# Kernel tuning notes

Measured on AMD Instinct MI355X. Metric: run time of the kernel, lower is better.

## Reference

```python
import jax, jax.numpy as jnp
import numpy as np

S, B, D_MODEL, H, DH = 2048, 2, 1024, 16, 64
FACTOR = 1.0 / np.sqrt(DH).astype(np.float32)


def setup_inputs() -> dict:
    key = jax.random.key(0)
    ks = jax.random.split(key, 12)
    sc = 0.02
    inp = {
        'query': jax.random.normal(ks[0], (S, B, D_MODEL), jnp.float32),
        'key': jax.random.normal(ks[1], (S, B, D_MODEL), jnp.float32),
        'value': jax.random.normal(ks[2], (S, B, D_MODEL), jnp.float32),
        # causal mask [seq_q, seq_k, 1]; 0 -> masked
        'mask': jnp.tril(jnp.ones((S, S), dtype=bool))[:, :, None],
        'Wq': jax.random.normal(ks[3], (H * DH, D_MODEL), jnp.float32) * sc,
        'bq': jnp.zeros((H * DH,), jnp.float32),
        'Wk': jax.random.normal(ks[4], (H * DH, D_MODEL), jnp.float32) * sc,
        'bk': jnp.zeros((H * DH,), jnp.float32),
        'Wv': jax.random.normal(ks[5], (H * DH, D_MODEL), jnp.float32) * sc,
        'bv': jnp.zeros((H * DH,), jnp.float32),
        'Wo': jax.random.normal(ks[6], (D_MODEL, H * DH), jnp.float32) * sc,
        'bo': jnp.zeros((D_MODEL,), jnp.float32),
    }
    return inp


def _split_heads(x):
    # pattern: 's b (head_dim head_num) -> s b head_num head_dim' (head_dim is OUTER)
    s, b, _ = x.shape
    return x.reshape(s, b, DH, H).transpose(0, 1, 3, 2)  # [s,b,H,DH]


def reference(query, key, value, mask, Wq, bq, Wk, bk, Wv, bv, Wo, bo):
    q = _split_heads(query @ Wq.T + bq)
    k = _split_heads(key @ Wk.T + bk)
    v = _split_heads(value @ Wv.T + bv)
    scores = jnp.einsum('ibhd,jbhd->ijbh', q, k) * FACTOR  # [i,j,b,h]
    scores = jnp.where(mask[..., None], scores, -jnp.inf)
    attn = jax.nn.softmax(scores, axis=1)  # softmax over keys (dim=1)
    out = jnp.einsum('ijbh,jbhd->ibhd', attn, v)  # [i,b,h,d]
    out = out.reshape(S, B, H * DH)  # 'i b h d -> i b (h d)'
    return out @ Wo.T + bo
```

## Files before the change

kernel.cpp:

```cpp
#include <hip/hip_runtime.h>


typedef float f32x4 __attribute__((ext_vector_type(4)));
typedef float f32x16 __attribute__((ext_vector_type(16)));
typedef __bf16 bf16x8_t __attribute__((ext_vector_type(8)));
typedef unsigned short ushort8 __attribute__((ext_vector_type(8)));
typedef unsigned int uint4v __attribute__((ext_vector_type(4)));
typedef unsigned int uint2v __attribute__((ext_vector_type(2)));

#define S_LEN 2048
#define BATCH 2
#define DMODEL 1024
#define NHEAD 16
#define DHEAD 64
#define K_SCALE 0.18033688011112042f
#define NCHUNK 51

__device__ __forceinline__ unsigned short f2bf(float x) {
  unsigned int u = __builtin_bit_cast(unsigned int, x);
  u += 0x7fffu + ((u >> 16) & 1u);
  return (unsigned short)(u >> 16);
}

__device__ __forceinline__ f32x4 mfma16(ushort8 a, ushort8 b, f32x4 c) {
  return __builtin_amdgcn_mfma_f32_16x16x32_bf16(
      __builtin_bit_cast(bf16x8_t, a), __builtin_bit_cast(bf16x8_t, b), c, 0, 0, 0);
}
__device__ __forceinline__ f32x16 mfma32(ushort8 a, ushort8 b, f32x16 c) {
  return __builtin_amdgcn_mfma_f32_32x32x16_bf16(
      __builtin_bit_cast(bf16x8_t, a), __builtin_bit_cast(bf16x8_t, b), c, 0, 0, 0);
}

__device__ __forceinline__ float max3f(float a, float b, float c) {
  return fmaxf(fmaxf(a, b), c);
}

__device__ __forceinline__ ushort8 pack8(float4 a, float4 b, float s) {
  ushort8 t;
  t[0] = f2bf(a.x * s); t[1] = f2bf(a.y * s); t[2] = f2bf(a.z * s); t[3] = f2bf(a.w * s);
  t[4] = f2bf(b.x * s); t[5] = f2bf(b.y * s); t[6] = f2bf(b.z * s); t[7] = f2bf(b.w * s);
  return t;
}

__device__ __forceinline__ void gload16(unsigned short* lds, const unsigned short* g) {
  __builtin_amdgcn_global_load_lds(
      (const __attribute__((address_space(1))) unsigned int*)g,
      (__attribute__((address_space(3))) unsigned int*)lds, 16, 0, 0);
}

__global__ __launch_bounds__(256) void cvt_kernel(
    const float* __restrict__ q, const float* __restrict__ k, const float* __restrict__ v,
    const float* __restrict__ wq, const float* __restrict__ wk,
    const float* __restrict__ wv, const float* __restrict__ wo,
    unsigned short* __restrict__ qB, unsigned short* __restrict__ kB,
    unsigned short* __restrict__ vB, unsigned short* __restrict__ wqB,
    unsigned short* __restrict__ wkB, unsigned short* __restrict__ wvB,
    unsigned short* __restrict__ woB)
{
  const int c = blockIdx.x * 256 + threadIdx.x;
  const float* s; unsigned short* d; int base;
  if      (c < 524288)  { s = q;  d = qB;  base = 0; }
  else if (c < 1048576) { s = k;  d = kB;  base = 524288; }
  else if (c < 1572864) { s = v;  d = vB;  base = 1048576; }
  else if (c < 1703936) { s = wq; d = wqB; base = 1572864; }
  else if (c < 1835008) { s = wk; d = wkB; base = 1703936; }
  else if (c < 1966080) { s = wv; d = wvB; base = 1835008; }
  else                  { s = wo; d = woB; base = 1966080; }
  const size_t off = (size_t)(c - base) * 8;
  const float4 v0 = *reinterpret_cast<const float4*>(s + off);
  const float4 v1 = *reinterpret_cast<const float4*>(s + off + 4);
  *reinterpret_cast<ushort8*>(d + off) = pack8(v0, v1, 1.0f);
}

__global__ __launch_bounds__(256) void gemm_qkv_kernel(
    const unsigned short* __restrict__ qA, const unsigned short* __restrict__ kA,
    const unsigned short* __restrict__ vA,
    const unsigned short* __restrict__ wqW, const unsigned short* __restrict__ wkW,
    const unsigned short* __restrict__ wvW,
    const float* __restrict__ bq, const float* __restrict__ bk,
    const float* __restrict__ bv,
    unsigned short* __restrict__ Cq, unsigned short* __restrict__ Ck,
    unsigned short* __restrict__ Cv)
{
  __shared__ __align__(16) unsigned short As[2][128 * 64];
  __shared__ __align__(16) unsigned short Ws[2][64 * 64];
  const int z = blockIdx.z;
  const unsigned short* A = (z == 0) ? qA : (z == 1) ? kA : vA;
  const unsigned short* W = (z == 0) ? wqW : (z == 1) ? wkW : wvW;
  const float* bias = (z == 0) ? bq : (z == 1) ? bk : bv;
  unsigned short* C = (z == 0) ? Cq : (z == 1) ? Ck : Cv;
  const float oscale = (z == 1) ? K_SCALE : 1.0f;

  const int tid = threadIdx.x;
  const int lane = tid & 63;
  const int w = tid >> 6;
  const int wm = (w >> 1) * 64, wn = (w & 1) * 32;
  const int g = lane >> 4, lr = lane & 15;

  const int bid = (int)blockIdx.x;
  const int widx = (bid & 7) * 64 + (bid >> 3);
  const int n0 = (widx & 15) * 64;
  const int m0 = (widx >> 4) * 128;

  f32x4 acc[4][2] = {};

#define STAGE(buf, k0)                                                              \
  {                                                                                 \
    _Pragma("unroll")                                                               \
    for (int ii = 0; ii < 4; ++ii) {                                                \
      const int c = ii * 256 + tid;                                                 \
      const int row = c >> 3;                                                       \
      const int sl = (c & 7) ^ (row & 7);                                           \
      gload16(&As[buf][c * 8], A + (size_t)(m0 + row) * DMODEL + (k0) + sl * 8);    \
    }                                                                               \
    _Pragma("unroll")                                                               \
    for (int ii = 0; ii < 2; ++ii) {                                                \
      const int c = ii * 256 + tid;                                                 \
      const int row = c >> 3;                                                       \
      const int sl = (c & 7) ^ (row & 7);                                           \
      gload16(&Ws[buf][c * 8], W + (size_t)(n0 + row) * DMODEL + (k0) + sl * 8);    \
    }                                                                               \
  }

  STAGE(0, 0);
  int cur = 0;

  for (int t = 0; t < 16; ++t) {
    __syncthreads();
    if (t < 15) STAGE(cur ^ 1, (t + 1) * 64);

    const char* ab = (const char*)&As[cur][0];
    const char* wb = (const char*)&Ws[cur][0];
#pragma unroll
    for (int kk = 0; kk < 2; ++kk) {
      ushort8 af[4], bw[2];
#pragma unroll
      for (int mt = 0; mt < 4; ++mt) {
        const int row = wm + mt * 16 + lr;
        af[mt] = *reinterpret_cast<const ushort8*>(
            ab + row * 128 + (((kk * 4 + g) ^ (row & 7)) << 4));
      }
#pragma unroll
      for (int nt = 0; nt < 2; ++nt) {
        const int row = wn + nt * 16 + lr;
        bw[nt] = *reinterpret_cast<const ushort8*>(
            wb + row * 128 + (((kk * 4 + g) ^ (row & 7)) << 4));
      }
      __builtin_amdgcn_s_setprio(1);
#pragma unroll
      for (int mt = 0; mt < 4; ++mt)
#pragma unroll
        for (int nt = 0; nt < 2; ++nt)
          acc[mt][nt] = mfma16(af[mt], bw[nt], acc[mt][nt]);
      __builtin_amdgcn_s_setprio(0);
    }
    cur ^= 1;
  }
#undef STAGE

  __syncthreads();
  unsigned short* T = &As[0][0];
#pragma unroll
  for (int nt = 0; nt < 2; ++nt) {
    const int col = n0 + wn + nt * 16 + lr;
    const float bvv = bias[col];
#pragma unroll
    for (int mt = 0; mt < 4; ++mt)
#pragma unroll
      for (int r = 0; r < 4; ++r) {
        const int lrow = wm + mt * 16 + g * 4 + r;
        T[lrow * 64 + wn + nt * 16 + lr] = f2bf((acc[mt][nt][r] + bvv) * oscale);
      }
  }
  __syncthreads();

  const int dfirst = n0 >> 4;
  if (z < 2) {
#pragma unroll
    for (int it = 0; it < 8; ++it) {
      const int e = it * 256 + tid;
      const int h = e & 15, lrow = e >> 4;
      const int n = m0 + lrow, s = n >> 1, bb = n & 1;
      const unsigned short v0 = T[lrow * 64 + 0 * 16 + h];
      const unsigned short v1 = T[lrow * 64 + 1 * 16 + h];
      const unsigned short v2 = T[lrow * 64 + 2 * 16 + h];
      const unsigned short v3 = T[lrow * 64 + 3 * 16 + h];
      uint2v pk = { (unsigned)v0 | ((unsigned)v1 << 16),
                    (unsigned)v2 | ((unsigned)v3 << 16) };
      *reinterpret_cast<uint2v*>(
          C + ((size_t)(bb * 16 + h) * S_LEN + s) * DHEAD + dfirst) = pk;
    }
  } else {
    const int run = tid >> 1, shalf = tid & 1;
    const int bb = run >> 6, rem = run & 63;
    const int h = rem >> 2, dl = rem & 3;
    const int sbase = (m0 >> 1) + shalf * 32;
    unsigned short vals[32];
#pragma unroll
    for (int i = 0; i < 32; ++i) {
      const int lrow = (shalf * 32 + i) * 2 + bb;
      vals[i] = T[lrow * 64 + dl * 16 + h];
    }
    unsigned short* dstp =
        C + ((size_t)(bb * 16 + h) * DHEAD + dfirst + dl) * S_LEN + sbase;
#pragma unroll
    for (int seg = 0; seg < 4; ++seg) {
      uint4v pk;
#pragma unroll
      for (int j = 0; j < 4; ++j)
        pk[j] = (unsigned)vals[seg * 8 + 2 * j] |
                ((unsigned)vals[seg * 8 + 2 * j + 1] << 16);
      *reinterpret_cast<uint4v*>(dstp + seg * 8) = pk;
    }
  }
}

__global__ __launch_bounds__(256) void gemm_out_kernel(
    const unsigned short* __restrict__ A, const unsigned short* __restrict__ W,
    const float* __restrict__ bias, float* __restrict__ C)
{
  __shared__ __align__(16) unsigned short As[2][128 * 64];
  __shared__ __align__(16) unsigned short Ws[2][64 * 64];
  const int tid = threadIdx.x;
  const int lane = tid & 63;
  const int w = tid >> 6;
  const int wm = (w >> 1) * 64, wn = (w & 1) * 32;
  const int g = lane >> 4, lr = lane & 15;

  const int bid = (int)blockIdx.x;
  const int widx = (bid & 7) * 64 + (bid >> 3);
  const int n0 = (widx & 15) * 64;
  const int m0 = (widx >> 4) * 128;

  f32x4 acc[4][2] = {};

#define STAGE(buf, k0)                                                              \
  {                                                                                 \
    _Pragma("unroll")                                                               \
    for (int ii = 0; ii < 4; ++ii) {                                                \
      const int c = ii * 256 + tid;                                                 \
      const int row = c >> 3;                                                       \
      const int sl = (c & 7) ^ (row & 7);                                           \
      gload16(&As[buf][c * 8], A + (size_t)(m0 + row) * DMODEL + (k0) + sl * 8);    \
    }                                                                               \
    _Pragma("unroll")                                                               \
    for (int ii = 0; ii < 2; ++ii) {                                                \
      const int c = ii * 256 + tid;                                                 \
      const int row = c >> 3;                                                       \
      const int sl = (c & 7) ^ (row & 7);                                           \
      gload16(&Ws[buf][c * 8], W + (size_t)(n0 + row) * DMODEL + (k0) + sl * 8);    \
    }                                                                               \
  }

  STAGE(0, 0);
  int cur = 0;

  for (int t = 0; t < 16; ++t) {
    __syncthreads();
    if (t < 15) STAGE(cur ^ 1, (t + 1) * 64);

    const char* ab = (const char*)&As[cur][0];
    const char* wb = (const char*)&Ws[cur][0];
#pragma unroll
    for (int kk = 0; kk < 2; ++kk) {
      ushort8 af[4], bw[2];
#pragma unroll
      for (int mt = 0; mt < 4; ++mt) {
        const int row = wm + mt * 16 + lr;
        af[mt] = *reinterpret_cast<const ushort8*>(
            ab + row * 128 + (((kk * 4 + g) ^ (row & 7)) << 4));
      }
#pragma unroll
      for (int nt = 0; nt < 2; ++nt) {
        const int row = wn + nt * 16 + lr;
        bw[nt] = *reinterpret_cast<const ushort8*>(
            wb + row * 128 + (((kk * 4 + g) ^ (row & 7)) << 4));
      }
      __builtin_amdgcn_s_setprio(1);
#pragma unroll
      for (int mt = 0; mt < 4; ++mt)
#pragma unroll
        for (int nt = 0; nt < 2; ++nt)
          acc[mt][nt] = mfma16(af[mt], bw[nt], acc[mt][nt]);
      __builtin_amdgcn_s_setprio(0);
    }
    cur ^= 1;
  }
#undef STAGE

#pragma unroll
  for (int nt = 0; nt < 2; ++nt) {
    const int col = n0 + wn + nt * 16 + lr;
    const float bvv = bias[col];
#pragma unroll
    for (int mt = 0; mt < 4; ++mt)
#pragma unroll
      for (int r = 0; r < 4; ++r) {
        const int rowg = m0 + wm + mt * 16 + g * 4 + r;
        C[(size_t)rowg * DMODEL + col] = acc[mt][nt][r] + bvv;
      }
  }
}

__global__ __launch_bounds__(256, 4) void attn_part_kernel(
    const unsigned short* __restrict__ Qh, const unsigned short* __restrict__ Kh,
    const unsigned short* __restrict__ Vh, unsigned short* __restrict__ Opart,
    float* __restrict__ mlbuf)
{
  __shared__ __align__(16) unsigned short Ks[2][64 * 64];
  __shared__ __align__(16) unsigned short Vs[2][64 * 64];

  const int tid = threadIdx.x;
  const int lane = tid & 63;
  const int w = tid >> 6;
  const int ln31 = lane & 31;
  const int hf = lane >> 5;

  const int bid = (int)blockIdx.x;
  const int xcd = bid & 7;
  const int sl8 = bid >> 3;
  const int hb = xcd * 4 + sl8 / NCHUNK;
  const int chunkid = sl8 % NCHUNK;

  int u = chunkid;
  int Q = 0, nc = 1;
  while (u >= nc) { u -= nc; ++Q; nc = Q / 3 + 1; }
  const int c = u;

  const int head = hb & 15, b = hb >> 4;
  const int slot = hb * NCHUNK + chunkid;
  const int t0 = c * 6;
  const int tmax = 2 * Q + 1;
  const int t1 = (tmax < t0 + 5) ? tmax : (t0 + 5);
  const int q0 = Q * 128;

  const size_t hoff = (size_t)(b * NHEAD + head) * (S_LEN * DHEAD);
  const unsigned short* Qg = Qh + hoff;
  const unsigned short* Kg = Kh + hoff;
  const unsigned short* Vg = Vh + hoff;

  const int qwb = q0 + w * 32;
  const int qg = qwb + ln31;

  ushort8 qf[4];
#pragma unroll
  for (int kt = 0; kt < 4; ++kt)
    qf[kt] = *reinterpret_cast<const ushort8*>(Qg + (size_t)qg * DHEAD + kt * 16 + hf * 8);

  f32x16 oa0 = {0}, oa1 = {0};
  float mrun = -1e30f, ssum = 0.f;

#define STAGE(buf, kv)                                                             \
  {                                                                                \
    _Pragma("unroll")                                                              \
    for (int ii = 0; ii < 2; ++ii) {                                               \
      const int c2 = ii * 256 + tid;                                               \
      const int row = c2 >> 3;                                                     \
      const int sl = (c2 & 7) ^ (row & 7);                                         \
      gload16(&Ks[buf][c2 * 8], Kg + (size_t)((kv) + row) * 64 + sl * 8);          \
    }                                                                              \
    _Pragma("unroll")                                                              \
    for (int ii = 0; ii < 2; ++ii) {                                               \
      const int c2 = ii * 256 + tid;                                               \
      const int row = c2 >> 3;                                                     \
      const int sl = (c2 & 7) ^ (row & 7);                                         \
      gload16(&Vs[buf][c2 * 8], Vg + (size_t)row * S_LEN + (kv) + sl * 8);         \
    }                                                                              \
  }

  STAGE(0, t0 * 64);
  int cur = 0;

  const int kb0 = ln31 * 128 + ((hf * 16) ^ ((ln31 & 7) << 4));
  const int kb1 = (32 + ln31) * 128 + ((hf * 16) ^ ((ln31 & 7) << 4));

  for (int t = t0; t <= t1; ++t) {
    const int kv0 = t * 64;
    __syncthreads();
    if (t < t1) STAGE(cur ^ 1, kv0 + 64);

    if (kv0 <= qwb + 31) {
      f32x16 sc0 = {0}, sc1 = {0};
      {
        const char* ksb = (const char*)&Ks[cur][0];
        __builtin_amdgcn_s_setprio(1);
#pragma unroll
        for (int kt = 0; kt < 4; ++kt) {
          ushort8 kf0 = *reinterpret_cast<const ushort8*>(ksb + (kb0 ^ (kt << 5)));
          ushort8 kf1 = *reinterpret_cast<const ushort8*>(ksb + (kb1 ^ (kt << 5)));
          sc0 = mfma32(kf0, qf[kt], sc0);
          sc1 = mfma32(kf1, qf[kt], sc1);
        }
        __builtin_amdgcn_s_setprio(0);
      }

      if (kv0 + 63 > qwb) {
#pragma unroll
        for (int r = 0; r < 16; ++r) {
          const int keyb = kv0 + (r & 3) + 8 * (r >> 2) + 4 * hf;
          if (keyb > qg) sc0[r] = -1e30f;
          if (keyb + 32 > qg) sc1[r] = -1e30f;
        }
      }

      float m0a = max3f(sc0[0], sc0[1], sc0[2]);
      float m1a = max3f(sc0[3], sc0[4], sc0[5]);
      float m2a = max3f(sc0[6], sc0[7], sc0[8]);
      float m3a = max3f(sc0[9], sc0[10], sc0[11]);
      float m4a = max3f(sc0[12], sc0[13], sc0[14]);
      float m5a = max3f(sc0[15], sc1[0], sc1[1]);
      float m6a = max3f(sc1[2], sc1[3], sc1[4]);
      float m7a = max3f(sc1[5], sc1[6], sc1[7]);
      float m8a = max3f(sc1[8], sc1[9], sc1[10]);
      float m9a = max3f(sc1[11], sc1[12], sc1[13]);
      float mAa = fmaxf(sc1[14], sc1[15]);
      float n0a = max3f(m0a, m1a, m2a);
      float n1a = max3f(m3a, m4a, m5a);
      float n2a = max3f(m6a, m7a, m8a);
      float n3a = fmaxf(m9a, mAa);
      float pmax = fmaxf(max3f(n0a, n1a, n2a), n3a);
      pmax = fmaxf(pmax, __shfl_xor(pmax, 32, 64));

      if (!__all(pmax <= mrun + 8.0f)) {
        const float mnew = fmaxf(mrun, pmax);
        const float scl = exp2f(mrun - mnew);
        ssum *= scl;
#pragma unroll
        for (int r = 0; r < 16; ++r) { oa0[r] *= scl; oa1[r] *= scl; }
        mrun = mnew;
      }

      float pv0[16], pv1[16];
#pragma unroll
      for (int r = 0; r < 16; ++r) {
        pv0[r] = exp2f(sc0[r] - mrun);
        pv1[r] = exp2f(sc1[r] - mrun);
      }
      float a8[8];
#pragma unroll
      for (int r = 0; r < 8; ++r)
        a8[r] = (pv0[r] + pv0[r + 8]) + (pv1[r] + pv1[r + 8]);
      float a4_0 = a8[0] + a8[4], a4_1 = a8[1] + a8[5];
      float a4_2 = a8[2] + a8[6], a4_3 = a8[3] + a8[7];
      float psum = (a4_0 + a4_1) + (a4_2 + a4_3);
      psum += __shfl_xor(psum, 32, 64);
      ssum += psum;

      unsigned int cc[16];
#pragma unroll
      for (int j = 0; j < 8; ++j) {
        asm("v_cvt_pk_bf16_f32 %0, %1, %2" : "=v"(cc[j]) : "v"(pv0[2 * j]), "v"(pv0[2 * j + 1]));
        asm("v_cvt_pk_bf16_f32 %0, %1, %2" : "=v"(cc[8 + j]) : "v"(pv1[2 * j]), "v"(pv1[2 * j + 1]));
      }

      uint4v pfw[4];
#pragma unroll
      for (int mt = 0; mt < 2; ++mt) {
#pragma unroll
        for (int ktl = 0; ktl < 2; ++ktl) {
          const int o = mt * 8 + ktl * 4;
          unsigned x0 = cc[o + 0], x2 = cc[o + 2];
          unsigned y0 = cc[o + 1], y2 = cc[o + 3];
          asm("v_permlane32_swap_b32 %0, %1" : "+v"(x0), "+v"(x2));
          asm("v_permlane32_swap_b32 %0, %1" : "+v"(y0), "+v"(y2));
          uint4v u4;
          u4[0] = x0; u4[1] = y0; u4[2] = x2; u4[3] = y2;
          pfw[mt * 2 + ktl] = u4;
        }
      }

      {
        const char* vsb = (const char*)&Vs[cur][0];
        __builtin_amdgcn_s_setprio(1);
#pragma unroll
        for (int kt = 0; kt < 4; ++kt) {
          ushort8 vf0 = *reinterpret_cast<const ushort8*>(vsb + (kb0 ^ (kt << 5)));
          ushort8 vf1 = *reinterpret_cast<const ushort8*>(vsb + (kb1 ^ (kt << 5)));
          ushort8 pfr = __builtin_bit_cast(ushort8, pfw[kt]);
          oa0 = mfma32(vf0, pfr, oa0);
          oa1 = mfma32(vf1, pfr, oa1);
        }
        __builtin_amdgcn_s_setprio(0);
      }
    }

    cur ^= 1;
  }
#undef STAGE

  const int ql = w * 32 + ln31;
  unsigned short* ob = Opart + (size_t)slot * 8192 + ql * 64;
#pragma unroll
  for (int mt2 = 0; mt2 < 2; ++mt2) {
#pragma unroll
    for (int rq = 0; rq < 4; ++rq) {
      const int dd = mt2 * 32 + 8 * rq + 4 * hf;
      const f32x16& a = mt2 ? oa1 : oa0;
      unsigned int w0, w1;
      asm("v_cvt_pk_bf16_f32 %0, %1, %2" : "=v"(w0)
          : "v"(a[4 * rq + 0]), "v"(a[4 * rq + 1]));
      asm("v_cvt_pk_bf16_f32 %0, %1, %2" : "=v"(w1)
          : "v"(a[4 * rq + 2]), "v"(a[4 * rq + 3]));
      uint2v pk = { w0, w1 };
      *reinterpret_cast<uint2v*>(ob + dd) = pk;
    }
  }
  if (hf == 0) {
    mlbuf[slot * 256 + ql] = mrun;
    mlbuf[slot * 256 + 128 + ql] = ssum;
  }
}

__global__ __launch_bounds__(256) void attn_combine_kernel(
    const unsigned short* __restrict__ Opart, const float* __restrict__ mlbuf,
    unsigned short* __restrict__ O)
{
  const int Q = blockIdx.x, hb = blockIdx.y;
  const int head = hb & 15, b = hb >> 4;
  const int nch = Q / 3 + 1;
  int off = 0;
  for (int j = 0; j < Q; ++j) off += j / 3 + 1;
  const int s0 = hb * NCHUNK + off;

  const int tid = threadIdx.x;
  const int q = tid >> 1, dh = (tid & 1) * 32;

  float mc[6], lc[6];
  float M = -1e30f;
  for (int cc = 0; cc < nch; ++cc) {
    mc[cc] = mlbuf[(s0 + cc) * 256 + q];
    lc[cc] = mlbuf[(s0 + cc) * 256 + 128 + q];
    M = fmaxf(M, mc[cc]);
  }
  float L = 0.f, wgt[6];
  for (int cc = 0; cc < nch; ++cc) {
    wgt[cc] = exp2f(mc[cc] - M);
    L += wgt[cc] * lc[cc];
  }
  const float invL = 1.0f / L;

  float acc[32] = {};
  for (int cc = 0; cc < nch; ++cc) {
    const unsigned short* p = Opart + (size_t)(s0 + cc) * 8192 + q * 64 + dh;
    const float wv = wgt[cc];
#pragma unroll
    for (int seg = 0; seg < 4; ++seg) {
      ushort8 v = *reinterpret_cast<const ushort8*>(p + seg * 8);
#pragma unroll
      for (int j = 0; j < 8; ++j) {
        const float f = __builtin_bit_cast(float, ((unsigned int)v[j]) << 16);
        acc[seg * 8 + j] += wv * f;
      }
    }
  }

  unsigned int wpk[16];
#pragma unroll
  for (int j = 0; j < 16; ++j) {
    asm("v_cvt_pk_bf16_f32 %0, %1, %2" : "=v"(wpk[j])
        : "v"(acc[2 * j] * invL), "v"(acc[2 * j + 1] * invL));
  }
  unsigned short* dst = O + ((size_t)((Q * 128 + q) * BATCH + b)) * DMODEL + head * DHEAD + dh;
#pragma unroll
  for (int seg = 0; seg < 4; ++seg)
    *reinterpret_cast<uint4v*>(dst + seg * 8) =
        uint4v{ wpk[4 * seg], wpk[4 * seg + 1], wpk[4 * seg + 2], wpk[4 * seg + 3] };
}

extern "C" void kernel_launch(void* const* d_in, const int* in_sizes, int n_in,
                              void* d_out, int out_size, void* d_ws, size_t ws_size,
                              hipStream_t stream)
{
  (void)in_sizes; (void)n_in; (void)out_size; (void)ws_size;
  const float* query = (const float*)d_in[0];
  const float* key_  = (const float*)d_in[1];
  const float* value = (const float*)d_in[2];
  const float* Wq = (const float*)d_in[4];
  const float* bq = (const float*)d_in[5];
  const float* Wk = (const float*)d_in[6];
  const float* bk = (const float*)d_in[7];
  const float* Wv = (const float*)d_in[8];
  const float* bv = (const float*)d_in[9];
  const float* Wo = (const float*)d_in[10];
  const float* bo = (const float*)d_in[11];
  float* out = (float*)d_out;

  const size_t NE = (size_t)4096 * DMODEL;
  const size_t NW = (size_t)DMODEL * DMODEL;
  unsigned short* qB  = (unsigned short*)d_ws;
  unsigned short* kB  = qB + NE;
  unsigned short* vB  = kB + NE;
  unsigned short* g1  = vB + NE;
  unsigned short* Qhm = g1 + NE;
  unsigned short* Khm = Qhm + NE;
  unsigned short* Vdm = Khm + NE;
  unsigned short* wqB = Vdm + NE;
  unsigned short* wkB = wqB + NW;
  unsigned short* wvB = wkB + NW;
  unsigned short* woB = wvB + NW;
  unsigned short* Opart = qB;
  float* mlbuf = (float*)(Opart + (size_t)(NCHUNK * 32) * 8192);

  cvt_kernel<<<dim3(8192), 256, 0, stream>>>(query, key_, value, Wq, Wk, Wv, Wo,
                                             qB, kB, vB, wqB, wkB, wvB, woB);
  gemm_qkv_kernel<<<dim3(512, 1, 3), 256, 0, stream>>>(
      qB, kB, vB, wqB, wkB, wvB, bq, bk, bv, Qhm, Khm, Vdm);
  attn_part_kernel<<<dim3(NCHUNK * 32), 256, 0, stream>>>(Qhm, Khm, Vdm, Opart, mlbuf);
  attn_combine_kernel<<<dim3(16, 32), 256, 0, stream>>>(Opart, mlbuf, Qhm);
  gemm_out_kernel<<<dim3(512), 256, 0, stream>>>(Qhm, woB, bo, out);
}
```

Baseline: 135.6 us.

## Load K/V fragments directly from global memory in attention, pad GEMM transpose tile

The attention kernel drops its double-buffered LDS staging of K and V tiles and the per-tile __syncthreads. Each wave now reads its MFMA K and V fragments straight from global memory, and V loads are issued early so they overlap the softmax math. Waves also break out of the loop once past their causal range, and the occupancy hint in launch_bounds is removed. Separately, the QKV GEMM epilogue pads the LDS transpose tile stride to 65 to reduce bank conflicts. The risk is that each wave now refetches K/V from global or L2 instead of sharing it across waves through LDS.

After: 175.6 us. 29.5% more time.

```diff
diff --git a/kernel.cpp b/kernel.cpp
--- a/kernel.cpp
+++ b/kernel.cpp
@@ -15,6 +15,7 @@
 #define DHEAD 64
 #define K_SCALE 0.18033688011112042f
 #define NCHUNK 51
+#define TSTR 65
 
 __device__ __forceinline__ unsigned short f2bf(float x) {
   unsigned int u = __builtin_bit_cast(unsigned int, x);
@@ -169,7 +170,7 @@
 #pragma unroll
       for (int r = 0; r < 4; ++r) {
         const int lrow = wm + mt * 16 + g * 4 + r;
-        T[lrow * 64 + wn + nt * 16 + lr] = f2bf((acc[mt][nt][r] + bvv) * oscale);
+        T[lrow * TSTR + wn + nt * 16 + lr] = f2bf((acc[mt][nt][r] + bvv) * oscale);
       }
   }
   __syncthreads();
@@ -181,10 +182,10 @@
       const int e = it * 256 + tid;
       const int h = e & 15, lrow = e >> 4;
       const int n = m0 + lrow, s = n >> 1, bb = n & 1;
-      const unsigned short v0 = T[lrow * 64 + 0 * 16 + h];
-      const unsigned short v1 = T[lrow * 64 + 1 * 16 + h];
-      const unsigned short v2 = T[lrow * 64 + 2 * 16 + h];
-      const unsigned short v3 = T[lrow * 64 + 3 * 16 + h];
+      const unsigned short v0 = T[lrow * TSTR + 0 * 16 + h];
+      const unsigned short v1 = T[lrow * TSTR + 1 * 16 + h];
+      const unsigned short v2 = T[lrow * TSTR + 2 * 16 + h];
+      const unsigned short v3 = T[lrow * TSTR + 3 * 16 + h];
       uint2v pk = { (unsigned)v0 | ((unsigned)v1 << 16),
                     (unsigned)v2 | ((unsigned)v3 << 16) };
       *reinterpret_cast<uint2v*>(
@@ -199,7 +200,7 @@
 #pragma unroll
     for (int i = 0; i < 32; ++i) {
       const int lrow = (shalf * 32 + i) * 2 + bb;
-      vals[i] = T[lrow * 64 + dl * 16 + h];
+      vals[i] = T[lrow * TSTR + dl * 16 + h];
     }
     unsigned short* dstp =
         C + ((size_t)(bb * 16 + h) * DHEAD + dfirst + dl) * S_LEN + sbase;
@@ -302,14 +303,11 @@
   }
 }
 
-__global__ __launch_bounds__(256, 4) void attn_part_kernel(
+__global__ __launch_bounds__(256) void attn_part_kernel(
     const unsigned short* __restrict__ Qh, const unsigned short* __restrict__ Kh,
     const unsigned short* __restrict__ Vh, unsigned short* __restrict__ Opart,
     float* __restrict__ mlbuf)
 {
-  __shared__ __align__(16) unsigned short Ks[2][64 * 64];
-  __shared__ __align__(16) unsigned short Vs[2][64 * 64];
-
   const int tid = threadIdx.x;
   const int lane = tid & 63;
   const int w = tid >> 6;
@@ -350,143 +348,131 @@
   f32x16 oa0 = {0}, oa1 = {0};
   float mrun = -1e30f, ssum = 0.f;
 
-#define STAGE(buf, kv)                                                             \
-  {                                                                                \
-    _Pragma("unroll")                                                              \
-    for (int ii = 0; ii < 2; ++ii) {                                               \
-      const int c2 = ii * 256 + tid;                                               \
-      const int row = c2 >> 3;                                                     \
-      const int sl = (c2 & 7) ^ (row & 7);                                         \
-      gload16(&Ks[buf][c2 * 8], Kg + (size_t)((kv) + row) * 64 + sl * 8);          \
-    }                                                                              \
-    _Pragma("unroll")                                                              \
-    for (int ii = 0; ii < 2; ++ii) {                                               \
-      const int c2 = ii * 256 + tid;                                               \
-      const int row = c2 >> 3;                                                     \
-      const int sl = (c2 & 7) ^ (row & 7);                                         \
-      gload16(&Vs[buf][c2 * 8], Vg + (size_t)row * S_LEN + (kv) + sl * 8);         \
-    }                                                                              \
-  }
-
-  STAGE(0, t0 * 64);
-  int cur = 0;
-
-  const int kb0 = ln31 * 128 + ((hf * 16) ^ ((ln31 & 7) << 4));
-  const int kb1 = (32 + ln31) * 128 + ((hf * 16) ^ ((ln31 & 7) << 4));
+  const unsigned short* kp = Kg + (size_t)ln31 * DHEAD + hf * 8;
+  const unsigned short* vp = Vg + (size_t)ln31 * S_LEN + hf * 8;
 
   for (int t = t0; t <= t1; ++t) {
     const int kv0 = t * 64;
-    __syncthreads();
-    if (t < t1) STAGE(cur ^ 1, kv0 + 64);
-
-    if (kv0 <= qwb + 31) {
-      f32x16 sc0 = {0}, sc1 = {0};
-      {
-        const char* ksb = (const char*)&Ks[cur][0];
-        __builtin_amdgcn_s_setprio(1);
-#pragma unroll
-        for (int kt = 0; kt < 4; ++kt) {
-          ushort8 kf0 = *reinterpret_cast<const ushort8*>(ksb + (kb0 ^ (kt << 5)));
-          ushort8 kf1 = *reinterpret_cast<const ushort8*>(ksb + (kb1 ^ (kt << 5)));
-          sc0 = mfma32(kf0, qf[kt], sc0);
-          sc1 = mfma32(kf1, qf[kt], sc1);
-        }
-        __builtin_amdgcn_s_setprio(0);
-      }
-
-      if (kv0 + 63 > qwb) {
-#pragma unroll
-        for (int r = 0; r < 16; ++r) {
-          const int keyb = kv0 + (r & 3) + 8 * (r >> 2) + 4 * hf;
-          if (keyb > qg) sc0[r] = -1e30f;
-          if (keyb + 32 > qg) sc1[r] = -1e30f;
-        }
-      }
-
-      float m0a = max3f(sc0[0], sc0[1], sc0[2]);
-      float m1a = max3f(sc0[3], sc0[4], sc0[5]);
-      float m2a = max3f(sc0[6], sc0[7], sc0[8]);
-      float m3a = max3f(sc0[9], sc0[10], sc0[11]);
-      float m4a = max3f(sc0[12], sc0[13], sc0[14]);
-      float m5a = max3f(sc0[15], sc1[0], sc1[1]);
-      float m6a = max3f(sc1[2], sc1[3], sc1[4]);
-      float m7a = max3f(sc1[5], sc1[6], sc1[7]);
-      float m8a = max3f(sc1[8], sc1[9], sc1[10]);
-      float m9a = max3f(sc1[11], sc1[12], sc1[13]);
-      float mAa = fmaxf(sc1[14], sc1[15]);
-      float n0a = max3f(m0a, m1a, m2a);
-      float n1a = max3f(m3a, m4a, m5a);
-      float n2a = max3f(m6a, m7a, m8a);
-      float n3a = fmaxf(m9a, mAa);
-      float pmax = fmaxf(max3f(n0a, n1a, n2a), n3a);
-      pmax = fmaxf(pmax, __shfl_xor(pmax, 32, 64));
-
-      if (!__all(pmax <= mrun + 8.0f)) {
-        const float mnew = fmaxf(mrun, pmax);
-        const float scl = exp2f(mrun - mnew);
-        ssum *= scl;
-#pragma unroll
-        for (int r = 0; r < 16; ++r) { oa0[r] *= scl; oa1[r] *= scl; }
-        mrun = mnew;
-      }
-
-      float pv0[16], pv1[16];
+    if (kv0 > qwb + 31) break;
+
+    const unsigned short* kb = kp + (size_t)kv0 * DHEAD;
+    const unsigned short* vb = vp + kv0;
+
+    f32x16 sc0 = {0}, sc1 = {0};
+    {
+      __builtin_amdgcn_s_setprio(1);
+#pragma unroll
+      for (int kt = 0; kt < 4; ++kt) {
+        ushort8 kf0 = *reinterpret_cast<const ushort8*>(kb + kt * 16);
+        ushort8 kf1 = *reinterpret_cast<const ushort8*>(kb + 32 * DHEAD + kt * 16);
+        sc0 = mfma32(kf0, qf[kt], sc0);
+        sc1 = mfma32(kf1, qf[kt], sc1);
+      }
+      __builtin_amdgcn_s_setprio(0);
+    }
+
+    ushort8 vf0a, vf0b, vf0c, vf0d, vf1a, vf1b, vf1c, vf1d;
+    vf0a = *reinterpret_cast<const ushort8*>(vb + 0 * 16);
+    vf1a = *reinterpret_cast<const ushort8*>(vb + (size_t)32 * S_LEN + 0 * 16);
+    vf0b = *reinterpret_cast<const ushort8*>(vb + 1 * 16);
+    vf1b = *reinterpret_cast<const ushort8*>(vb + (size_t)32 * S_LEN + 1 * 16);
+    vf0c = *reinterpret_cast<const ushort8*>(vb + 2 * 16);
+    vf1c = *reinterpret_cast<const ushort8*>(vb + (size_t)32 * S_LEN + 2 * 16);
+    vf0d = *reinterpret_cast<const ushort8*>(vb + 3 * 16);
+    vf1d = *reinterpret_cast<const ushort8*>(vb + (size_t)32 * S_LEN + 3 * 16);
+
+    if (kv0 + 63 > qwb) {
 #pragma unroll
       for (int r = 0; r < 16; ++r) {
-        pv0[r] = exp2f(sc0[r] - mrun);
-        pv1[r] = exp2f(sc1[r] - mrun);
-      }
-      float a8[8];
-#pragma unroll
-      for (int r = 0; r < 8; ++r)
-        a8[r] = (pv0[r] + pv0[r + 8]) + (pv1[r] + pv1[r + 8]);
-      float a4_0 = a8[0] + a8[4], a4_1 = a8[1] + a8[5];
-      float a4_2 = a8[2] + a8[6], a4_3 = a8[3] + a8[7];
-      float psum = (a4_0 + a4_1) + (a4_2 + a4_3);
-      psum += __shfl_xor(psum, 32, 64);
-      ssum += psum;
-
-      unsigned int cc[16];
-#pragma unroll
-      for (int j = 0; j < 8; ++j) {
-        asm("v_cvt_pk_bf16_f32 %0, %1, %2" : "=v"(cc[j]) : "v"(pv0[2 * j]), "v"(pv0[2 * j + 1]));
-        asm("v_cvt_pk_bf16_f32 %0, %1, %2" : "=v"(cc[8 + j]) : "v"(pv1[2 * j]), "v"(pv1[2 * j + 1]));
-      }
-
-      uint4v pfw[4];
-#pragma unroll
-      for (int mt = 0; mt < 2; ++mt) {
-#pragma unroll
-        for (int ktl = 0; ktl < 2; ++ktl) {
-          const int o = mt * 8 + ktl * 4;
-          unsigned x0 = cc[o + 0], x2 = cc[o + 2];
-          unsigned y0 = cc[o + 1], y2 = cc[o + 3];
-          asm("v_permlane32_swap_b32 %0, %1" : "+v"(x0), "+v"(x2));
-          asm("v_permlane32_swap_b32 %0, %1" : "+v"(y0), "+v"(y2));
-          uint4v u4;
-          u4[0] = x0; u4[1] = y0; u4[2] = x2; u4[3] = y2;
-          pfw[mt * 2 + ktl] = u4;
-        }
-      }
-
-      {
-        const char* vsb = (const char*)&Vs[cur][0];
-        __builtin_amdgcn_s_setprio(1);
-#pragma unroll
-        for (int kt = 0; kt < 4; ++kt) {
-          ushort8 vf0 = *reinterpret_cast<const ushort8*>(vsb + (kb0 ^ (kt << 5)));
-          ushort8 vf1 = *reinterpret_cast<const ushort8*>(vsb + (kb1 ^ (kt << 5)));
-          ushort8 pfr = __builtin_bit_cast(ushort8, pfw[kt]);
-          oa0 = mfma32(vf0, pfr, oa0);
-          oa1 = mfma32(vf1, pfr, oa1);
-        }
-        __builtin_amdgcn_s_setprio(0);
-      }
-    }
-
-    cur ^= 1;
-  }
-#undef STAGE
+        const int keyb = kv0 + (r & 3) + 8 * (r >> 2) + 4 * hf;
+        if (keyb > qg) sc0[r] = -1e30f;
+        if (keyb + 32 > qg) sc1[r] = -1e30f;
+      }
+    }
+
+    float m0a = max3f(sc0[0], sc0[1], sc0[2]);
+    float m1a = max3f(sc0[3], sc0[4], sc0[5]);
+    float m2a = max3f(sc0[6], sc0[7], sc0[8]);
+    float m3a = max3f(sc0[9], sc0[10], sc0[11]);
+    float m4a = max3f(sc0[12], sc0[13], sc0[14]);
+    float m5a = max3f(sc0[15], sc1[0], sc1[1]);
+    float m6a = max3f(sc1[2], sc1[3], sc1[4]);
+    float m7a = max3f(sc1[5], sc1[6], sc1[7]);
+    float m8a = max3f(sc1[8], sc1[9], sc1[10]);
+    float m9a = max3f(sc1[11], sc1[12], sc1[13]);
+    float mAa = fmaxf(sc1[14], sc1[15]);
+    float n0a = max3f(m0a, m1a, m2a);
+    float n1a = max3f(m3a, m4a, m5a);
+    float n2a = max3f(m6a, m7a, m8a);
+    float n3a = fmaxf(m9a, mAa);
+    float pmax = fmaxf(max3f(n0a, n1a, n2a), n3a);
+    pmax = fmaxf(pmax, __shfl_xor(pmax, 32, 64));
+
+    if (!__all(pmax <= mrun + 8.0f)) {
+      const float mnew = fmaxf(mrun, pmax);
+      const float scl = exp2f(mrun - mnew);
+      ssum *= scl;
+#pragma unroll
+      for (int r = 0; r < 16; ++r) { oa0[r] *= scl; oa1[r] *= scl; }
+      mrun = mnew;
+    }
+
+    float pv0[16], pv1[16];
+#pragma unroll
+    for (int r = 0; r < 16; ++r) {
+      pv0[r] = exp2f(sc0[r] - mrun);
+      pv1[r] = exp2f(sc1[r] - mrun);
+    }
+    float a8[8];
+#pragma unroll
+    for (int r = 0; r < 8; ++r)
+      a8[r] = (pv0[r] + pv0[r + 8]) + (pv1[r] + pv1[r + 8]);
+    float a4_0 = a8[0] + a8[4], a4_1 = a8[1] + a8[5];
+    float a4_2 = a8[2] + a8[6], a4_3 = a8[3] + a8[7];
+    float psum = (a4_0 + a4_1) + (a4_2 + a4_3);
+    psum += __shfl_xor(psum, 32, 64);
+    ssum += psum;
+
+    unsigned int cc[16];
+#pragma unroll
+    for (int j = 0; j < 8; ++j) {
+      asm("v_cvt_pk_bf16_f32 %0, %1, %2" : "=v"(cc[j]) : "v"(pv0[2 * j]), "v"(pv0[2 * j + 1]));
+      asm("v_cvt_pk_bf16_f32 %0, %1, %2" : "=v"(cc[8 + j]) : "v"(pv1[2 * j]), "v"(pv1[2 * j + 1]));
+    }
+
+    uint4v pfw[4];
+#pragma unroll
+    for (int mt = 0; mt < 2; ++mt) {
+#pragma unroll
+      for (int ktl = 0; ktl < 2; ++ktl) {
+        const int o = mt * 8 + ktl * 4;
+        unsigned x0 = cc[o + 0], x2 = cc[o + 2];
+        unsigned y0 = cc[o + 1], y2 = cc[o + 3];
+        asm("v_permlane32_swap_b32 %0, %1" : "+v"(x0), "+v"(x2));
+        asm("v_permlane32_swap_b32 %0, %1" : "+v"(y0), "+v"(y2));
+        uint4v u4;
+        u4[0] = x0; u4[1] = y0; u4[2] = x2; u4[3] = y2;
+        pfw[mt * 2 + ktl] = u4;
+      }
+    }
+
+    {
+      __builtin_amdgcn_s_setprio(1);
+      ushort8 p0 = __builtin_bit_cast(ushort8, pfw[0]);
+      ushort8 p1 = __builtin_bit_cast(ushort8, pfw[1]);
+      ushort8 p2 = __builtin_bit_cast(ushort8, pfw[2]);
+      ushort8 p3 = __builtin_bit_cast(ushort8, pfw[3]);
+      oa0 = mfma32(vf0a, p0, oa0);
+      oa1 = mfma32(vf1a, p0, oa1);
+      oa0 = mfma32(vf0b, p1, oa0);
+      oa1 = mfma32(vf1b, p1, oa1);
+      oa0 = mfma32(vf0c, p2, oa0);
+      oa1 = mfma32(vf1c, p2, oa1);
+      oa0 = mfma32(vf0d, p3, oa0);
+      oa1 = mfma32(vf1d, p3, oa1);
+      __builtin_amdgcn_s_setprio(0);
+    }
+  }
 
   const int ql = w * 32 + ln31;
   unsigned short* ob = Opart + (size_t)slot * 8192 + ql * 64;
```
